# Optimization experiments

Hardware: AMD Instinct MI355X
Metric: run time of the kernel (lower is better)

The kernel has to match this reference:

```python
import jax, jax.numpy as jnp
import numpy as np
import math

DIM = 2048
N_HEADS = 16
HEAD_DIM = 128
BATCH = 2
T = 2048
EPS = 1e-5


def setup_inputs() -> dict:
    key = jax.random.key(0)
    ks = jax.random.split(key, 16)
    s = lambda fan_in: 1.0 / math.sqrt(fan_in)
    d = {}
    d['x'] = jax.random.normal(ks[0], (BATCH, T, DIM), dtype=jnp.float32)
    d['start_pos'] = 0
    # attention projections (weights stored [in, out])
    d['wq'] = jax.random.uniform(ks[1], (DIM, N_HEADS * HEAD_DIM), minval=-s(DIM), maxval=s(DIM))
    d['bq'] = jnp.zeros((N_HEADS * HEAD_DIM,), jnp.float32)
    d['wk'] = jax.random.uniform(ks[2], (DIM, HEAD_DIM), minval=-s(DIM), maxval=s(DIM))
    d['bk'] = jnp.zeros((HEAD_DIM,), jnp.float32)
    d['wv'] = jax.random.uniform(ks[3], (DIM, HEAD_DIM), minval=-s(DIM), maxval=s(DIM))
    d['bv'] = jnp.zeros((HEAD_DIM,), jnp.float32)
    d['wo'] = jax.random.uniform(ks[4], (N_HEADS * HEAD_DIM, DIM), minval=-s(N_HEADS * HEAD_DIM), maxval=s(N_HEADS * HEAD_DIM))
    d['bo'] = jnp.zeros((DIM,), jnp.float32)
    # layernorms
    d['ln1_g'] = jnp.ones((DIM,), jnp.float32)
    d['ln1_b'] = jnp.zeros((DIM,), jnp.float32)
    d['ln2_g'] = jnp.ones((DIM,), jnp.float32)
    d['ln2_b'] = jnp.zeros((DIM,), jnp.float32)
    # MLP (dim -> 4*dim -> dim), dropout p=0 is a no-op
    d['w1'] = jax.random.uniform(ks[5], (DIM, 4 * DIM), minval=-s(DIM), maxval=s(DIM))
    d['b1'] = jnp.zeros((4 * DIM,), jnp.float32)
    d['w2'] = jax.random.uniform(ks[6], (4 * DIM, DIM), minval=-s(4 * DIM), maxval=s(4 * DIM))
    d['b2'] = jnp.zeros((DIM,), jnp.float32)
    return d


def _layernorm(h, g, b):
    mu = jnp.mean(h, axis=-1, keepdims=True)
    var = jnp.mean(jnp.square(h - mu), axis=-1, keepdims=True)
    return (h - mu) * jax.lax.rsqrt(var + EPS) * g + b


def reference(x, start_pos, wq, bq, wk, bk, wv, bv, wo, bo, ln1_g, ln1_b, ln2_g, ln2_b, w1, b1, w2, b2):
    B, Tq, D = x.shape
    hd = wk.shape[1]
    H = wq.shape[1] // hd
    # --- MQA attention on pre-LN input (prefill: no kv cache) ---
    h = _layernorm(x, ln1_g, ln1_b)
    q = (h @ wq + bq).reshape(B, Tq, H, hd)          # [B,T,H,hd]
    k = h @ wk + bk                                   # [B,T,hd] single shared head
    v = h @ wv + bv                                   # [B,T,hd]
    scores = jnp.einsum('bthc,bsc->bhts', q, k) / math.sqrt(hd)
    causal = jnp.where(jnp.tril(jnp.ones((Tq, Tq), dtype=bool)), 0.0, -jnp.inf).astype(scores.dtype)
    attn = jax.nn.softmax(scores + causal, axis=-1)   # [B,H,T,T]
    ctx = jnp.einsum('bhts,bsc->bthc', attn, v).reshape(B, Tq, H * hd)
    out = ctx @ wo + bo
    x = x + out
    # --- GELU MLP (exact erf gelu, torch default) ---
    h2 = _layernorm(x, ln2_g, ln2_b)
    x = x + jax.nn.gelu(h2 @ w1 + b1, approximate=False) @ w2 + b2
    k_cat = k[:, None]                                # [B,1,T,hd]
    v_cat = v[:, None]
    return (x, k_cat, v_cat)
```

## Files before the change

kernel.cpp:

```cpp
#include <hip/hip_runtime.h>
#include <stdint.h>

#define DIMSZ 2048
#define HD 128
#define NH 16
#define BATCH 2
#define SEQ 2048
#define MROWS (BATCH*SEQ)
#define FFDIM (4*DIMSZ)
#define NQKV (DIMSZ + 2*HD)

typedef float f32x4 __attribute__((ext_vector_type(4)));
typedef __bf16 bf16x8 __attribute__((ext_vector_type(8)));
typedef __bf16 bf16x2 __attribute__((ext_vector_type(2)));
typedef _Float16 f16x8 __attribute__((ext_vector_type(8)));
typedef __bf16 bf16_t;
typedef _Float16 f16_t;

__device__ __forceinline__ void async16(const void* g, void* l) {
  __builtin_amdgcn_global_load_lds(
      (const __attribute__((address_space(1))) void*)(uintptr_t)g,
      (__attribute__((address_space(3))) void*)(uint32_t)(uintptr_t)l,
      16, 0, 0);
}

__device__ __forceinline__ float gelu_f(float x) {
  return 0.5f * x * (1.0f + erff(x * 0.70710678118654752f));
}

__device__ __forceinline__ void hard_barrier() {
  asm volatile("" ::: "memory");
  __builtin_amdgcn_s_barrier();
  asm volatile("" ::: "memory");
}

__global__ __launch_bounds__(256)
void k_trall(const float* __restrict__ wq, const float* __restrict__ wk,
             const float* __restrict__ wv, const float* __restrict__ wo,
             const float* __restrict__ w1, const float* __restrict__ w2,
             bf16_t* __restrict__ wqkvT, bf16_t* __restrict__ woT,
             bf16_t* __restrict__ w1T, bf16_t* __restrict__ w2T) {
  int bid = blockIdx.x;
  const float* src; bf16_t* dst; int R, C, t0;
  if (bid < 1024)      { src = wq; dst = wqkvT;                        R = 2048; C = 2048; t0 = bid; }
  else if (bid < 1088) { src = wk; dst = wqkvT + (size_t)2048 * 2048;  R = 2048; C = 128;  t0 = bid - 1024; }
  else if (bid < 1152) { src = wv; dst = wqkvT + (size_t)2176 * 2048;  R = 2048; C = 128;  t0 = bid - 1088; }
  else if (bid < 2176) { src = wo; dst = woT;                          R = 2048; C = 2048; t0 = bid - 1152; }
  else if (bid < 6272) { src = w1; dst = w1T;                          R = 2048; C = 8192; t0 = bid - 2176; }
  else                 { src = w2; dst = w2T;                          R = 8192; C = 2048; t0 = bid - 6272; }
  int tc = C >> 6;
  int c0 = (t0 % tc) * 64, r0 = (t0 / tc) * 64;
  __shared__ float tile[64][65];
  int lc = threadIdx.x & 63, lrow = threadIdx.x >> 6;
#pragma unroll
  for (int i = 0; i < 64; i += 4)
    tile[lrow + i][lc] = src[(size_t)(r0 + lrow + i) * C + c0 + lc];
  __syncthreads();
  int rp = threadIdx.x & 31, wc = threadIdx.x >> 5;
#pragma unroll
  for (int i = 0; i < 64; i += 8) {
    int c = wc + i;
    bf16x2 pk = {(bf16_t)tile[2 * rp][c], (bf16_t)tile[2 * rp + 1][c]};
    *(bf16x2*)(dst + (size_t)(c0 + c) * R + r0 + 2 * rp) = pk;
  }
}

__global__ __launch_bounds__(256)
void k_transpose_v(const bf16_t* __restrict__ v, bf16_t* __restrict__ vt) {
  __shared__ bf16_t tile[32][33];
  int b = blockIdx.z;
  int t0 = blockIdx.x * 32, d0 = blockIdx.y * 32;
  int tx = threadIdx.x & 31, ty = threadIdx.x >> 5;
#pragma unroll
  for (int i = 0; i < 32; i += 8)
    tile[ty + i][tx] = v[((size_t)(b * SEQ + t0 + ty + i)) * HD + d0 + tx];
  __syncthreads();
#pragma unroll
  for (int i = 0; i < 32; i += 8)
    vt[((size_t)(b * HD + d0 + ty + i)) * SEQ + t0 + tx] = tile[tx][ty + i];
}

__global__ __launch_bounds__(256)
void k_layernorm(const float* __restrict__ x, const float* __restrict__ g,
                 const float* __restrict__ bb, bf16_t* __restrict__ out) {
  int row = blockIdx.x;
  const float* xr = x + (size_t)row * DIMSZ;
  int t = threadIdx.x;
  float vals[8];
  float s = 0.f, s2 = 0.f;
#pragma unroll
  for (int i = 0; i < 8; ++i) {
    float v = xr[t + i * 256];
    vals[i] = v; s += v; s2 += v * v;
  }
#pragma unroll
  for (int o = 1; o < 64; o <<= 1) { s += __shfl_xor(s, o); s2 += __shfl_xor(s2, o); }
  __shared__ float red[8];
  if ((t & 63) == 0) { red[t >> 6] = s; red[4 + (t >> 6)] = s2; }
  __syncthreads();
  s = red[0] + red[1] + red[2] + red[3];
  s2 = red[4] + red[5] + red[6] + red[7];
  float mu = s * (1.0f / DIMSZ);
  float rstd = rsqrtf(s2 * (1.0f / DIMSZ) - mu * mu + 1e-5f);
  bf16_t* orow = out + (size_t)row * DIMSZ;
#pragma unroll
  for (int i = 0; i < 8; ++i) {
    int c = t + i * 256;
    orow[c] = (bf16_t)((vals[i] - mu) * rstd * g[c] + bb[c]);
  }
}

template <int FN>
__device__ __forceinline__ void gemm8_loop(
    const bf16_t* __restrict__ A, const bf16_t* __restrict__ BT,
    int ld, int Kloop, int bm, int bn, f32x4 (&acc)[8][FN], bf16_t* sh) {
  constexpr int BH = FN >> 1;
  constexpr int BN = FN * 64;
  const int tid = threadIdx.x;
  const int lane = tid & 63, lr = lane & 15, lg = lane >> 4;
  const int wave = tid >> 6, wm = wave >> 2, wn = wave & 3;
  bf16_t* const Ab0 = sh;
  bf16_t* const Bb0 = sh + 32768;
  const bf16_t* const Ag = A + (size_t)bm * 256 * ld;
  const bf16_t* const Bg = BT + (size_t)bn * BN * ld;

  auto stage = [&](const bf16_t* gbase, bf16_t* lbase, int h, int t) {
#pragma unroll
    for (int j = 0; j < 2; ++j) {
      int flat = (tid + j * 512) * 8;
      int r = flat >> 6, kp = flat & 63;
      int ks = kp ^ ((r & 7) << 3);
      async16(gbase + (size_t)(h * 128 + r) * ld + t * 64 + ks, lbase + flat);
    }
  };
  auto stA = [&](int c, int h, int t) { stage(Ag, Ab0 + (c * 2 + h) * 8192, h, t); };
  auto stB = [&](int c, int h, int t) { stage(Bg, Bb0 + (c * BH + h) * 8192, h, t); };

  const int xsw = (lr & 7) << 3;
  bf16x8 a_[4], b_[FN][2];
  auto lda4 = [&](int c, int m0, int kk) {
    const bf16_t* base = Ab0 + (c * 2 + wm) * 8192;
#pragma unroll
    for (int i = 0; i < 4; ++i)
      a_[i] = *(const bf16x8*)(base + ((m0 + i) * 16 + lr) * 64 + ((kk + lg * 8) ^ xsw));
  };
  auto ldb4 = [&](int c, int kx) {
#pragma unroll
    for (int nf = 0; nf < FN; ++nf) {
      int row = wn * (FN * 16) + nf * 16 + lr;
      const bf16_t* base =
          Bb0 + (c * BH + (BH == 2 ? (row >> 7) : 0)) * 8192 + (row & 127) * 64;
      b_[nf][kx] = *(const bf16x8*)(base + ((kx * 32 + lg * 8) ^ xsw));
    }
  };

#define LGKM0 asm volatile("s_waitcnt lgkmcnt(0)" ::: "memory");
#define VMC_GATE                                                     \
  if (BH == 2) { asm volatile("s_waitcnt vmcnt(4)" ::: "memory"); }  \
  else         { asm volatile("s_waitcnt vmcnt(2)" ::: "memory"); }
#define MFMA_Q(M0, KX)                                               \
  __builtin_amdgcn_s_setprio(1);                                     \
  _Pragma("unroll")                                                  \
  for (int i_ = 0; i_ < 4; ++i_)                                     \
    _Pragma("unroll")                                                \
    for (int nf = 0; nf < FN; ++nf)                                  \
      acc[(M0) + i_][nf] = __builtin_amdgcn_mfma_f32_16x16x32_bf16(  \
          a_[i_], b_[nf][KX], acc[(M0) + i_][nf], 0, 0, 0);          \
  __builtin_amdgcn_s_setprio(0);

  const int nit = Kloop >> 7;

  stA(0, 0, 0); stA(0, 1, 0);
  stB(0, 0, 0); if (BH == 2) stB(0, 1, 0);
  stB(1, 0, 1); if (BH == 2) stB(1, 1, 1);
  VMC_GATE;
  hard_barrier();

  for (int i = 0; i < nit; ++i) {
    const int t1 = 2 * i + 1, t2 = 2 * i + 2, t3 = 2 * i + 3;
    const bool g2 = (i < nit - 1);
    lda4(0, 0, 0); ldb4(0, 0);
    stA(1, 0, t1); stA(1, 1, t1);
    hard_barrier(); LGKM0;
    MFMA_Q(0, 0)
    hard_barrier();
    lda4(0, 4, 0); ldb4(0, 1);
    hard_barrier(); LGKM0;
    MFMA_Q(4, 0)
    hard_barrier();
    lda4(0, 0, 32);
    if (g2) { stB(0, 0, t2); if (BH == 2) stB(0, 1, t2); }
    hard_barrier(); LGKM0;
    MFMA_Q(0, 1)
    hard_barrier();
    lda4(0, 4, 32);
    if (i == nit - 1) { asm volatile("s_waitcnt vmcnt(0)" ::: "memory"); }
    else { VMC_GATE; }
    hard_barrier(); LGKM0;
    MFMA_Q(4, 1)
    hard_barrier();
    lda4(1, 0, 0); ldb4(1, 0);
    if (g2) { stA(0, 0, t2); stA(0, 1, t2); }
    hard_barrier(); LGKM0;
    MFMA_Q(0, 0)
    hard_barrier();
    lda4(1, 4, 0); ldb4(1, 1);
    hard_barrier(); LGKM0;
    MFMA_Q(4, 0)
    hard_barrier();
    lda4(1, 0, 32);
    if (g2) { stB(1, 0, t3); if (BH == 2) stB(1, 1, t3); }
    hard_barrier(); LGKM0;
    MFMA_Q(0, 1)
    hard_barrier();
    lda4(1, 4, 32);
    VMC_GATE;
    hard_barrier(); LGKM0;
    MFMA_Q(4, 1)
    hard_barrier();
  }
#undef LGKM0
#undef VMC_GATE
#undef MFMA_Q
}

__global__ __launch_bounds__(512, 1)
void k_oproj(const bf16_t* __restrict__ A, const bf16_t* __restrict__ BT,
             const float* __restrict__ bias, const float* __restrict__ res,
             float* __restrict__ outF) {
  extern __shared__ __align__(16) bf16_t sh8[];
  const int nt = DIMSZ / 128;
  int bm = blockIdx.x / nt, bn = blockIdx.x % nt;
  f32x4 acc[8][2] = {};
  gemm8_loop<2>(A, BT, DIMSZ, DIMSZ, bm, bn, acc, sh8);
  int tid = threadIdx.x, wave = tid >> 6, lane = tid & 63, lr = lane & 15, lg = lane >> 4;
  int wm = wave >> 2, wn = wave & 3;
  float* shF = (float*)sh8;
  int rl0 = wm * 128 + lg * 4;
  int cl0 = wn * 32 + lr;
#pragma unroll
  for (int nf = 0; nf < 2; ++nf) {
    int cl = cl0 + nf * 16;
    float bi = bias[bn * 128 + cl];
#pragma unroll
    for (int mf = 0; mf < 8; ++mf)
#pragma unroll
      for (int j = 0; j < 4; ++j)
        shF[(rl0 + mf * 16 + j) * 128 + cl] = acc[mf][nf][j] + bi;
  }
  hard_barrier();
  const float* rbase = res + (size_t)(bm * 256) * DIMSZ + bn * 128;
  float* gbase = outF + (size_t)(bm * 256) * DIMSZ + bn * 128;
#pragma unroll
  for (int s = 0; s < 16; ++s) {
    int flat = s * 512 + tid;
    int row = flat >> 5, cu = flat & 31;
    f32x4 v = *(const f32x4*)(shF + row * 128 + cu * 4);
    f32x4 r4 = *(const f32x4*)(rbase + (size_t)row * DIMSZ + cu * 4);
    *(f32x4*)(gbase + (size_t)row * DIMSZ + cu * 4) = v + r4;
  }
}

__global__ __launch_bounds__(512, 1)
void k_ffn1(const bf16_t* __restrict__ A, const bf16_t* __restrict__ BT,
            const float* __restrict__ bias, bf16_t* __restrict__ outB) {
  extern __shared__ __align__(16) bf16_t sh8[];
  const int nt = FFDIM / 256;
  int bm = blockIdx.x / nt, bn = blockIdx.x % nt;
  f32x4 acc[8][4] = {};
  gemm8_loop<4>(A, BT, DIMSZ, DIMSZ, bm, bn, acc, sh8);
  int tid = threadIdx.x, wave = tid >> 6, lane = tid & 63, lr = lane & 15, lg = lane >> 4;
  int wm = wave >> 2, wn = wave & 3;
  int rl0 = wm * 128 + lg * 4;
  int cl0 = wn * 64 + lr;
#pragma unroll
  for (int nf = 0; nf < 4; ++nf) {
    int cl = cl0 + nf * 16;
    float bi = bias[bn * 256 + cl];
#pragma unroll
    for (int mf = 0; mf < 8; ++mf)
#pragma unroll
      for (int j = 0; j < 4; ++j)
        sh8[(rl0 + mf * 16 + j) * 256 + cl] = (bf16_t)gelu_f(acc[mf][nf][j] + bi);
  }
  hard_barrier();
  bf16_t* gbase = outB + (size_t)(bm * 256) * FFDIM + bn * 256;
#pragma unroll
  for (int s = 0; s < 16; ++s) {
    int flat = s * 512 + tid;
    int row = flat >> 5, cu = flat & 31;
    f32x4 v = *(const f32x4*)(sh8 + row * 256 + cu * 8);
    *(f32x4*)(gbase + (size_t)row * FFDIM + cu * 8) = v;
  }
}

__global__ __launch_bounds__(512, 1)
void k_ffn2(const bf16_t* __restrict__ A, const bf16_t* __restrict__ BT,
            f16_t* __restrict__ p0, f16_t* __restrict__ p1) {
  extern __shared__ __align__(16) bf16_t sh8[];
  int swz = (blockIdx.x & 7) * 32 + (blockIdx.x >> 3);
  int kh = swz >> 7;
  int tile = swz & 127;
  int bm = tile >> 3, bn = tile & 7;
  f32x4 acc[8][4] = {};
  gemm8_loop<4>(A + kh * (FFDIM / 2), BT + kh * (FFDIM / 2), FFDIM, FFDIM / 2,
                bm, bn, acc, sh8);
  int tid = threadIdx.x, wave = tid >> 6, lane = tid & 63, lr = lane & 15, lg = lane >> 4;
  int wm = wave >> 2, wn = wave & 3;
  f16_t* shH = (f16_t*)sh8;
  int rl0 = wm * 128 + lg * 4;
  int cl0 = wn * 64 + lr;
#pragma unroll
  for (int nf = 0; nf < 4; ++nf) {
    int cl = cl0 + nf * 16;
#pragma unroll
    for (int mf = 0; mf < 8; ++mf)
#pragma unroll
      for (int j = 0; j < 4; ++j)
        shH[(rl0 + mf * 16 + j) * 256 + cl] = (f16_t)acc[mf][nf][j];
  }
  hard_barrier();
  f16_t* gbase = (kh ? p1 : p0) + (size_t)(bm * 256) * DIMSZ + bn * 256;
#pragma unroll
  for (int s = 0; s < 16; ++s) {
    int flat = s * 512 + tid;
    int row = flat >> 5, cu = flat & 31;
    f32x4 v = *(const f32x4*)(shH + row * 256 + cu * 8);
    *(f32x4*)(gbase + (size_t)row * DIMSZ + cu * 8) = v;
  }
}

__global__ __launch_bounds__(256)
void k_ffn2red(const f16_t* __restrict__ p0, const f16_t* __restrict__ p1,
               const float* __restrict__ b2, float* __restrict__ outx) {
  int row = blockIdx.x;
  int c0 = threadIdx.x * 8;
  size_t base = (size_t)row * DIMSZ + c0;
  f16x8 a = *(const f16x8*)(p0 + base);
  f16x8 b = *(const f16x8*)(p1 + base);
  f32x4 o0 = *(const f32x4*)(outx + base);
  f32x4 o1 = *(const f32x4*)(outx + base + 4);
  f32x4 b0 = *(const f32x4*)(b2 + c0);
  f32x4 b1 = *(const f32x4*)(b2 + c0 + 4);
#pragma unroll
  for (int i = 0; i < 4; ++i) {
    o0[i] += (float)a[i] + (float)b[i] + b0[i];
    o1[i] += (float)a[4 + i] + (float)b[4 + i] + b1[i];
  }
  *(f32x4*)(outx + base) = o0;
  *(f32x4*)(outx + base + 4) = o1;
}

__global__ __launch_bounds__(512, 1)
void k_qkv(const bf16_t* __restrict__ A, const bf16_t* __restrict__ BT,
           const float* __restrict__ bq, const float* __restrict__ bk,
           const float* __restrict__ bv,
           bf16_t* __restrict__ qb, float* __restrict__ outk,
           float* __restrict__ outv, bf16_t* __restrict__ kbf,
           bf16_t* __restrict__ vbf) {
  extern __shared__ __align__(16) bf16_t sh8[];
  const int nt = NQKV / 256;
  int bm = blockIdx.x / nt, bn = blockIdx.x % nt;
  f32x4 acc[8][4] = {};
  gemm8_loop<4>(A, BT, DIMSZ, DIMSZ, bm, bn, acc, sh8);
  int tid = threadIdx.x, wave = tid >> 6, lane = tid & 63, lr = lane & 15, lg = lane >> 4;
  int wm = wave >> 2, wn = wave & 3;
  int rl0 = wm * 128 + lg * 4;
  int cl0 = wn * 64 + lr;
#pragma unroll
  for (int nf = 0; nf < 4; ++nf) {
    int cl = cl0 + nf * 16;
    int cg = bn * 256 + cl;
    float bi = (cg < 2048) ? bq[cg] : (cg < 2176 ? bk[cg - 2048] : bv[cg - 2176]);
#pragma unroll
    for (int mf = 0; mf < 8; ++mf)
#pragma unroll
      for (int j = 0; j < 4; ++j) {
        float v = acc[mf][nf][j] + bi;
        sh8[(rl0 + mf * 16 + j) * 256 + cl] = (bf16_t)v;
        if (cg >= 2048) {
          int r = bm * 256 + rl0 + mf * 16 + j;
          if (cg < 2176) outk[(size_t)r * HD + (cg - 2048)] = v;
          else           outv[(size_t)r * HD + (cg - 2176)] = v;
        }
      }
  }
  hard_barrier();
#pragma unroll
  for (int s = 0; s < 16; ++s) {
    int flat = s * 512 + tid;
    int row = flat >> 5, cu = flat & 31;
    f32x4 v = *(const f32x4*)(sh8 + row * 256 + cu * 8);
    int r = bm * 256 + row;
    if (bn < 8) {
      *(f32x4*)(qb + (size_t)r * DIMSZ + bn * 256 + cu * 8) = v;
    } else {
      int ce = cu * 8;
      if (ce < 128) *(f32x4*)(kbf + (size_t)r * HD + ce) = v;
      else          *(f32x4*)(vbf + (size_t)r * HD + (ce - 128)) = v;
    }
  }
}

__global__ __launch_bounds__(256, 2)
void k_attn(const bf16_t* __restrict__ q, const bf16_t* __restrict__ k,
            const bf16_t* __restrict__ vt, bf16_t* __restrict__ ctx) {
  __shared__ __align__(16) bf16_t Ks[2][64 * 128];
  __shared__ __align__(16) bf16_t Vs[2][128 * 64];
  __shared__ bf16_t Pw[4][16][72];
  int pp = blockIdx.x, h = blockIdx.y, b = blockIdx.z;
  int tid = threadIdx.x, wave = tid >> 6, lane = tid & 63, lr = lane & 15, lg = lane >> 4;
  const bf16_t* kb = k + (size_t)b * SEQ * HD;
  const bf16_t* vb = vt + (size_t)b * HD * SEQ;

#define STAGE_TILE(buf, s0_)                                                      \
  {                                                                               \
    _Pragma("unroll")                                                             \
    for (int i = 0; i < 4; ++i) {                                                 \
      int flat = (i * 256 + tid) * 8;                                             \
      int kr = flat >> 7, kc = flat & 127;                                        \
      int ksrc = (((kc >> 3) ^ (kr & 7)) << 3) | (kc & 7);                        \
      async16(kb + (size_t)((s0_) + kr) * HD + ksrc, (void*)(Ks[buf] + flat));    \
      int vr = flat >> 6, vc = flat & 63;                                         \
      int vsrc = (((vc >> 3) ^ (vr & 7)) << 3) | (vc & 7);                        \
      async16(vb + (size_t)vr * SEQ + (s0_) + vsrc, (void*)(Vs[buf] + flat));     \
    }                                                                             \
  }

  for (int half = 0; half < 2; ++half) {
    int qt = half ? (31 - pp) : pp;
    int q0 = qt * 64;
    int qw = q0 + wave * 16;
    const bf16_t* qbase = q + ((size_t)(b * SEQ + qw + lr)) * DIMSZ + h * HD;
    bf16x8 qf[4];
#pragma unroll
    for (int kk = 0; kk < 4; ++kk) qf[kk] = *(const bf16x8*)(qbase + kk * 32 + lg * 8);
    f32x4 o[8] = {};
    float m_[4], l_[4];
#pragma unroll
    for (int j = 0; j < 4; ++j) { m_[j] = -3.0e38f; l_[j] = 0.f; }
    int qglob0 = qw + lg * 4;
    int ntiles = qt + 1;

    STAGE_TILE(0, 0)
    __syncthreads();
    for (int t = 0; t < ntiles; ++t) {
      int cur = t & 1;
      if (t + 1 < ntiles) STAGE_TILE(cur ^ 1, (t + 1) * 64)
      int s0 = t * 64;
      const bf16_t* Kc = Ks[cur];
      const bf16_t* Vc = Vs[cur];
      f32x4 sf[4] = {};
#pragma unroll
      for (int nf = 0; nf < 4; ++nf) {
        int R = nf * 16 + lr;
#pragma unroll
        for (int kk = 0; kk < 4; ++kk)
          sf[nf] = __builtin_amdgcn_mfma_f32_16x16x32_bf16(
              qf[kk],
              *(const bf16x8*)(Kc + R * 128 + (((kk * 4 + lg) ^ (R & 7)) << 3)),
              sf[nf], 0, 0, 0);
      }
#pragma unroll
      for (int nf = 0; nf < 4; ++nf) {
        int col = s0 + nf * 16 + lr;
#pragma unroll
        for (int j = 0; j < 4; ++j) {
          float v = sf[nf][j] * 0.088388347648318447f;
          sf[nf][j] = (col <= qglob0 + j) ? v : -3.0e38f;
        }
      }
      float mx[4];
#pragma unroll
      for (int j = 0; j < 4; ++j)
        mx[j] = fmaxf(fmaxf(sf[0][j], sf[1][j]), fmaxf(sf[2][j], sf[3][j]));
#pragma unroll
      for (int o_ = 1; o_ < 16; o_ <<= 1)
#pragma unroll
        for (int j = 0; j < 4; ++j) mx[j] = fmaxf(mx[j], __shfl_xor(mx[j], o_));
      float fsc[4], mn[4];
#pragma unroll
      for (int j = 0; j < 4; ++j) {
        mn[j] = fmaxf(m_[j], mx[j]);
        fsc[j] = __expf(m_[j] - mn[j]);
        m_[j] = mn[j];
      }
      float ps[4] = {0.f, 0.f, 0.f, 0.f};
#pragma unroll
      for (int nf = 0; nf < 4; ++nf)
#pragma unroll
        for (int j = 0; j < 4; ++j) {
          float pv = __expf(sf[nf][j] - mn[j]);
          ps[j] += pv;
          Pw[wave][lg * 4 + j][nf * 16 + lr] = (bf16_t)pv;
        }
#pragma unroll
      for (int o_ = 1; o_ < 16; o_ <<= 1)
#pragma unroll
        for (int j = 0; j < 4; ++j) ps[j] += __shfl_xor(ps[j], o_);
#pragma unroll
      for (int j = 0; j < 4; ++j) l_[j] = l_[j] * fsc[j] + ps[j];
#pragma unroll
      for (int df = 0; df < 8; ++df)
#pragma unroll
        for (int j = 0; j < 4; ++j) o[df][j] *= fsc[j];
      asm volatile("" ::: "memory");
      bf16x8 pa[2];
#pragma unroll
      for (int kk = 0; kk < 2; ++kk)
        pa[kk] = *(const bf16x8*)(&Pw[wave][lr][kk * 32 + lg * 8]);
#pragma unroll
      for (int df = 0; df < 8; ++df) {
        int R = df * 16 + lr;
#pragma unroll
        for (int kk = 0; kk < 2; ++kk)
          o[df] = __builtin_amdgcn_mfma_f32_16x16x32_bf16(
              pa[kk],
              *(const bf16x8*)(Vc + R * 64 + (((kk * 4 + lg) ^ (R & 7)) << 3)),
              o[df], 0, 0, 0);
      }
      __syncthreads();
    }
    bf16_t* cb = ctx + ((size_t)(b * SEQ + qw)) * DIMSZ + h * HD;
#pragma unroll
    for (int df = 0; df < 8; ++df)
#pragma unroll
      for (int j = 0; j < 4; ++j)
        cb[(size_t)(lg * 4 + j) * DIMSZ + df * 16 + lr] = (bf16_t)(o[df][j] / l_[j]);
  }
#undef STAGE_TILE
}

extern "C" void kernel_launch(void* const* d_in, const int* in_sizes, int n_in,
                              void* d_out, int out_size, void* d_ws, size_t ws_size,
                              hipStream_t stream) {
  const float* x   = (const float*)d_in[0];
  const float* wq  = (const float*)d_in[2];
  const float* bq  = (const float*)d_in[3];
  const float* wk  = (const float*)d_in[4];
  const float* bk  = (const float*)d_in[5];
  const float* wv  = (const float*)d_in[6];
  const float* bv  = (const float*)d_in[7];
  const float* wo  = (const float*)d_in[8];
  const float* bo  = (const float*)d_in[9];
  const float* g1  = (const float*)d_in[10];
  const float* be1 = (const float*)d_in[11];
  const float* g2  = (const float*)d_in[12];
  const float* be2 = (const float*)d_in[13];
  const float* w1  = (const float*)d_in[14];
  const float* bb1 = (const float*)d_in[15];
  const float* w2  = (const float*)d_in[16];
  const float* bb2 = (const float*)d_in[17];

  float* outx = (float*)d_out;
  float* outk = outx + (size_t)MROWS * DIMSZ;
  float* outv = outk + (size_t)MROWS * HD;

  char* p = (char*)d_ws;
  auto alloc = [&](size_t bytes) -> char* {
    char* r = p;
    p += (bytes + 255) & ~(size_t)255;
    return r;
  };
  bf16_t* wqkvT = (bf16_t*)alloc((size_t)NQKV * DIMSZ * 2);
  bf16_t* woT = (bf16_t*)alloc((size_t)DIMSZ * DIMSZ * 2);
  bf16_t* w1T = (bf16_t*)alloc((size_t)FFDIM * DIMSZ * 2);
  bf16_t* w2T = (bf16_t*)alloc((size_t)DIMSZ * FFDIM * 2);
  bf16_t* hb  = (bf16_t*)alloc((size_t)MROWS * DIMSZ * 2);
  bf16_t* qb  = (bf16_t*)alloc((size_t)MROWS * DIMSZ * 2);
  bf16_t* kbf = (bf16_t*)alloc((size_t)MROWS * HD * 2);
  bf16_t* vbf = (bf16_t*)alloc((size_t)MROWS * HD * 2);
  bf16_t* vtb = (bf16_t*)alloc((size_t)BATCH * HD * SEQ * 2);
  bf16_t* f1b = (bf16_t*)alloc((size_t)MROWS * FFDIM * 2);
  f16_t* p0  = (f16_t*)alloc((size_t)MROWS * DIMSZ * 2);
  f16_t* p1  = (f16_t*)alloc((size_t)MROWS * DIMSZ * 2);
  (void)ws_size; (void)in_sizes; (void)n_in; (void)out_size;

  dim3 blk(256);
  const int LDSG = 131072;
  k_trall<<<10368, blk, 0, stream>>>(wq, wk, wv, wo, w1, w2, wqkvT, woT, w1T, w2T);
  k_layernorm<<<MROWS, blk, 0, stream>>>(x, g1, be1, hb);
  k_qkv<<<(MROWS / 256) * (NQKV / 256), 512, LDSG, stream>>>(
      hb, wqkvT, bq, bk, bv, qb, outk, outv, kbf, vbf);
  k_transpose_v<<<dim3(SEQ / 32, HD / 32, BATCH), blk, 0, stream>>>(vbf, vtb);
  k_attn<<<dim3(SEQ / 64 / 2, NH, BATCH), blk, 0, stream>>>(qb, kbf, vtb, hb);
  k_oproj<<<(MROWS / 256) * (DIMSZ / 128), 512, LDSG, stream>>>(hb, woT, bo, x, outx);
  k_layernorm<<<MROWS, blk, 0, stream>>>(outx, g2, be2, qb);
  k_ffn1<<<(MROWS / 256) * (FFDIM / 256), 512, LDSG, stream>>>(qb, w1T, bb1, f1b);
  k_ffn2<<<256, 512, LDSG, stream>>>(f1b, w2T, p0, p1);
  k_ffn2red<<<MROWS, blk, 0, stream>>>(p0, p1, bb2, outx);
}
```

Baseline: 527.4 us.

## Restructure GEMM main loop schedule with fewer barriers and single B fragment

```diff
diff --git a/kernel.cpp b/kernel.cpp
--- a/kernel.cpp
+++ b/kernel.cpp
@@ -137,7 +137,7 @@
   auto stB = [&](int c, int h, int t) { stage(Bg, Bb0 + (c * BH + h) * 8192, h, t); };
 
   const int xsw = (lr & 7) << 3;
-  bf16x8 a_[4], b_[FN][2];
+  bf16x8 a_[4], b_[FN];
   auto lda4 = [&](int c, int m0, int kk) {
     const bf16_t* base = Ab0 + (c * 2 + wm) * 8192;
 #pragma unroll
@@ -150,76 +150,69 @@
       int row = wn * (FN * 16) + nf * 16 + lr;
       const bf16_t* base =
           Bb0 + (c * BH + (BH == 2 ? (row >> 7) : 0)) * 8192 + (row & 127) * 64;
-      b_[nf][kx] = *(const bf16x8*)(base + ((kx * 32 + lg * 8) ^ xsw));
+      b_[nf] = *(const bf16x8*)(base + ((kx * 32 + lg * 8) ^ xsw));
     }
   };
 
-#define LGKM0 asm volatile("s_waitcnt lgkmcnt(0)" ::: "memory");
 #define VMC_GATE                                                     \
-  if (BH == 2) { asm volatile("s_waitcnt vmcnt(4)" ::: "memory"); }  \
-  else         { asm volatile("s_waitcnt vmcnt(2)" ::: "memory"); }
-#define MFMA_Q(M0, KX)                                               \
+  if (BH == 2) { asm volatile("s_waitcnt vmcnt(8)" ::: "memory"); }  \
+  else         { asm volatile("s_waitcnt vmcnt(6)" ::: "memory"); }
+#define MFMA_Q(M0)                                                   \
   __builtin_amdgcn_s_setprio(1);                                     \
   _Pragma("unroll")                                                  \
   for (int i_ = 0; i_ < 4; ++i_)                                     \
     _Pragma("unroll")                                                \
     for (int nf = 0; nf < FN; ++nf)                                  \
       acc[(M0) + i_][nf] = __builtin_amdgcn_mfma_f32_16x16x32_bf16(  \
-          a_[i_], b_[nf][KX], acc[(M0) + i_][nf], 0, 0, 0);          \
+          a_[i_], b_[nf], acc[(M0) + i_][nf], 0, 0, 0);              \
   __builtin_amdgcn_s_setprio(0);
 
   const int nit = Kloop >> 7;
 
+  stB(0, 0, 0); if (BH == 2) stB(0, 1, 0);
   stA(0, 0, 0); stA(0, 1, 0);
-  stB(0, 0, 0); if (BH == 2) stB(0, 1, 0);
   stB(1, 0, 1); if (BH == 2) stB(1, 1, 1);
-  VMC_GATE;
-  hard_barrier();
 
   for (int i = 0; i < nit; ++i) {
-    const int t1 = 2 * i + 1, t2 = 2 * i + 2, t3 = 2 * i + 3;
+    const int t2 = 2 * i + 2, t3 = 2 * i + 3;
     const bool g2 = (i < nit - 1);
+    stA(1, 0, 2 * i + 1); stA(1, 1, 2 * i + 1);
+    VMC_GATE;
+    hard_barrier();
     lda4(0, 0, 0); ldb4(0, 0);
-    stA(1, 0, t1); stA(1, 1, t1);
-    hard_barrier(); LGKM0;
-    MFMA_Q(0, 0)
-    hard_barrier();
-    lda4(0, 4, 0); ldb4(0, 1);
-    hard_barrier(); LGKM0;
-    MFMA_Q(4, 0)
-    hard_barrier();
-    lda4(0, 0, 32);
+    MFMA_Q(0)
+    hard_barrier();
+    lda4(0, 4, 0);
+    MFMA_Q(4)
+    hard_barrier();
+    lda4(0, 0, 32); ldb4(0, 1);
+    MFMA_Q(0)
+    hard_barrier();
     if (g2) { stB(0, 0, t2); if (BH == 2) stB(0, 1, t2); }
-    hard_barrier(); LGKM0;
-    MFMA_Q(0, 1)
-    hard_barrier();
     lda4(0, 4, 32);
-    if (i == nit - 1) { asm volatile("s_waitcnt vmcnt(0)" ::: "memory"); }
-    else { VMC_GATE; }
-    hard_barrier(); LGKM0;
-    MFMA_Q(4, 1)
+    MFMA_Q(4)
+    hard_barrier();
+    if (g2) {
+      stA(0, 0, t2); stA(0, 1, t2);
+      VMC_GATE;
+    } else {
+      asm volatile("s_waitcnt vmcnt(0)" ::: "memory");
+    }
     hard_barrier();
     lda4(1, 0, 0); ldb4(1, 0);
-    if (g2) { stA(0, 0, t2); stA(0, 1, t2); }
-    hard_barrier(); LGKM0;
-    MFMA_Q(0, 0)
-    hard_barrier();
-    lda4(1, 4, 0); ldb4(1, 1);
-    hard_barrier(); LGKM0;
-    MFMA_Q(4, 0)
-    hard_barrier();
-    lda4(1, 0, 32);
+    MFMA_Q(0)
+    hard_barrier();
+    lda4(1, 4, 0);
+    MFMA_Q(4)
+    hard_barrier();
+    lda4(1, 0, 32); ldb4(1, 1);
+    MFMA_Q(0)
+    hard_barrier();
     if (g2) { stB(1, 0, t3); if (BH == 2) stB(1, 1, t3); }
-    hard_barrier(); LGKM0;
-    MFMA_Q(0, 1)
-    hard_barrier();
     lda4(1, 4, 32);
-    VMC_GATE;
-    hard_barrier(); LGKM0;
-    MFMA_Q(4, 1)
-    hard_barrier();
-  }
-#undef LGKM0
+    MFMA_Q(4)
+    hard_barrier();
+  }
 #undef VMC_GATE
 #undef MFMA_Q
 }
```

Measured after the change: 539.9 us. 2.4% more time.
